# Kernel optimization log

Measured on AMD Instinct MI355X. Metric: run time of the kernel, lower is better.

Reference implementation:

```python
import jax, jax.numpy as jnp
import numpy as np
from jax import lax

B, L, DIN, DOUT, K = 8, 4096, 256, 256, 3


def _gates(x, W, b, k):
    # x: [B, L, Din] -> conv over time, channels-first like torch Conv1d
    xt = jnp.transpose(x, (0, 2, 1))  # [B, Din, L]
    pad = (k - 1) // 2
    g = lax.conv_general_dilated(xt, W, window_strides=(1,), padding=[(pad, pad)],
                                 dimension_numbers=("NCH", "OIH", "NCH"))
    g = g + b[None, :, None]
    g = jnp.transpose(g, (0, 2, 1))  # [B, L, 3*Dout]
    f, o, z = jnp.split(g, 3, axis=-1)
    return jax.nn.sigmoid(f), jax.nn.sigmoid(o), jnp.tanh(z)


def _fo_pool(f, z, init_cell, reverse):
    # c_t = f_t * c_{t-1} + (1 - f_t) * z_t ; scan over time axis
    fT = jnp.transpose(f, (1, 0, 2))  # [L, B, D]
    zT = jnp.transpose(z, (1, 0, 2))

    def step(c, fz):
        ft, zt = fz
        c = ft * c + (1.0 - ft) * zt
        return c, c

    _, cells = lax.scan(step, init_cell, (fT, zT), reverse=reverse)
    return jnp.transpose(cells, (1, 0, 2))  # [B, L, D]


def setup_inputs() -> dict:
    key = jax.random.key(0)
    k1, k2, k3, k4, k5, k6 = jax.random.split(key, 6)
    scale_in = 1.0 / np.sqrt(DIN * K)
    inp = {
        "input": jax.random.normal(k1, (B, L, DIN), dtype=jnp.float32),
        "lengths": jnp.full((B,), L, dtype=jnp.int64) if False else jax.random.randint(k2, (B,), 1, L + 1),
        "W_fwd": jax.random.uniform(k3, (3 * DOUT, DIN, K), dtype=jnp.float32, minval=-scale_in, maxval=scale_in),
        "b_fwd": jax.random.uniform(k4, (3 * DOUT,), dtype=jnp.float32, minval=-scale_in, maxval=scale_in),
        "W_bwd": jax.random.uniform(k5, (3 * DOUT, DIN, K), dtype=jnp.float32, minval=-scale_in, maxval=scale_in),
        "b_bwd": jax.random.uniform(k6, (3 * DOUT,), dtype=jnp.float32, minval=-scale_in, maxval=scale_in),
    }
    return inp


def reference(input, lengths, W_fwd, b_fwd, W_bwd, b_bwd):
    init_cell = jnp.zeros((input.shape[0], DOUT), dtype=input.dtype)

    # forward direction
    f, o, z = _gates(input, W_fwd, b_fwd, K)
    cell = _fo_pool(f, z, init_cell, reverse=False)
    hidden = cell * o

    # backward direction
    fr, orr, zr = _gates(input, W_bwd, b_bwd, K)
    rcell = _fo_pool(fr, zr, init_cell, reverse=True)
    rhidden = rcell * orr

    output = jnp.concatenate([hidden, rhidden], axis=-1)  # [B, L, 2*Dout]
    last_h = jnp.concatenate([hidden[:, -1, :], rhidden[:, -1, :]], axis=-1)
    last_c = jnp.concatenate([cell[:, -1, :], rcell[:, -1, :]], axis=-1)
    return output, last_h, last_c
```

## Files before the change

kernel.cpp:

```cpp
#include <hip/hip_runtime.h>
#include <hip/hip_bf16.h>
#include <hip/hip_fp16.h>

#define B_     8
#define L_     4096
#define DIN    256
#define DOUT   256
#define NGATE  1536
#define KDIM   768
#define LP     (L_ + 2)
#define CHUNK  64
#define NCHUNK (L_ / CHUNK)

typedef short  short8  __attribute__((ext_vector_type(8)));
typedef __bf16 bf16x8  __attribute__((ext_vector_type(8)));
typedef float  floatx4 __attribute__((ext_vector_type(4)));

__device__ __forceinline__ float fast_sigmoid(float x) {
    return __builtin_amdgcn_rcpf(1.f + __expf(-x));
}
__device__ __forceinline__ float fast_tanh(float x) {
    return 1.f - 2.f * __builtin_amdgcn_rcpf(1.f + __expf(2.f * x));
}
__device__ __forceinline__ unsigned short f2bf(float x) {
    unsigned u = __float_as_uint(x);
    u += 0x7FFF + ((u >> 16) & 1);
    return (unsigned short)(u >> 16);
}
__device__ __forceinline__ void gload16(const unsigned short* g, unsigned short* l) {
    __builtin_amdgcn_global_load_lds((const __attribute__((address_space(1))) void*)g,
                                     (__attribute__((address_space(3))) void*)l,
                                     16, 0, 0);
}

__global__ void prep_x(const float* __restrict__ x, unsigned short* __restrict__ Xp) {
    int idx = blockIdx.x * 256 + threadIdx.x;
    int row = idx >> 6;
    if (row >= B_ * LP) return;
    int c4 = (idx & 63) << 2;
    int b = row / LP, r = row - b * LP;
    float4 v = make_float4(0.f, 0.f, 0.f, 0.f);
    if (r >= 1 && r <= L_) {
        v = *(const float4*)(x + ((size_t)(b * L_ + (r - 1))) * DIN + c4);
    }
    ushort4 o = make_ushort4(f2bf(v.x), f2bf(v.y), f2bf(v.z), f2bf(v.w));
    *(ushort4*)(Xp + (size_t)row * DIN + c4) = o;
}

__global__ void prep_w(const float* __restrict__ Wf, const float* __restrict__ bf_,
                       const float* __restrict__ Wb, const float* __restrict__ bb,
                       unsigned short* __restrict__ Wc, float* __restrict__ bc) {
    int gid = blockIdx.x * 256 + threadIdx.x;
    if (gid < NGATE) {
        bc[gid] = (gid < 768) ? bf_[gid] : bb[gid - 768];
    }
    if (gid >= NGATE * KDIM) return;
    int n = gid / KDIM, k = gid - n * KDIM;
    int s = k >> 8, ic = k & 255;
    const float* W = (n < 768) ? Wf : Wb;
    int oc = (n < 768) ? n : n - 768;
    float v = W[(size_t)oc * KDIM + ic * 3 + s];
    Wc[(size_t)n * KDIM + k] = f2bf(v);
}

__launch_bounds__(256)
__global__ void gemm_gates(const unsigned short* __restrict__ Xp,
                           const unsigned short* __restrict__ Wc,
                           const float* __restrict__ bc,
                           _Float16* __restrict__ gates) {
    __shared__ unsigned short As[128 * 64];
    __shared__ unsigned short Bs[128 * 64];
    const int tid  = threadIdx.x;
    const int lane = tid & 63, wave = tid >> 6;
    const int quad = lane >> 4, l16 = lane & 15;
    const int wr = wave >> 1, wcl = wave & 1;

    int flat = blockIdx.x;
    int xcd  = flat & 7;
    int slot = flat >> 3;
    int m    = xcd * 32 + slot / 12;
    int nblk = slot % 12;
    const int b  = m >> 5;
    const int t0 = (m & 31) << 7;
    const int n0 = nblk << 7;
    const unsigned short* Ab = Xp + (size_t)b * LP * DIN;

    int rowj[4], cgj[4];
#pragma unroll
    for (int j = 0; j < 4; j++) {
        int G = (wave * 4 + j) * 64 + lane;
        rowj[j] = G >> 3;
        cgj[j]  = ((G & 7) ^ (rowj[j] & 7)) * 8;
    }

    floatx4 acc[4][4];
#pragma unroll
    for (int i = 0; i < 4; i++)
#pragma unroll
        for (int j = 0; j < 4; j++) acc[i][j] = (floatx4)0.f;

    for (int k0 = 0; k0 < KDIM; k0 += 64) {
        const int sh = k0 >> 8;
        const int c0 = k0 & 255;
#pragma unroll
        for (int j = 0; j < 4; j++) {
            gload16(Ab + (size_t)(t0 + rowj[j] + sh) * DIN + c0 + cgj[j],
                    &As[(wave * 4 + j) * 512]);
            gload16(Wc + (size_t)(n0 + rowj[j]) * KDIM + k0 + cgj[j],
                    &Bs[(wave * 4 + j) * 512]);
        }
        __syncthreads();
#pragma unroll
        for (int kk = 0; kk < 2; kk++) {
            const int g0 = kk * 4 + quad;
            short8 af[4], bfr[4];
#pragma unroll
            for (int mi = 0; mi < 4; mi++) {
                int row = wr * 64 + mi * 16 + l16;
                af[mi] = *(const short8*)&As[row * 64 + ((g0 ^ (row & 7)) << 3)];
            }
#pragma unroll
            for (int ni = 0; ni < 4; ni++) {
                int row = wcl * 64 + ni * 16 + l16;
                bfr[ni] = *(const short8*)&Bs[row * 64 + ((g0 ^ (row & 7)) << 3)];
            }
#pragma unroll
            for (int mi = 0; mi < 4; mi++)
#pragma unroll
                for (int ni = 0; ni < 4; ni++)
                    acc[mi][ni] = __builtin_amdgcn_mfma_f32_16x16x32_bf16(
                        __builtin_bit_cast(bf16x8, af[mi]),
                        __builtin_bit_cast(bf16x8, bfr[ni]),
                        acc[mi][ni], 0, 0, 0);
        }
        __syncthreads();
    }

#pragma unroll
    for (int ni = 0; ni < 4; ni++) {
        int col = wcl * 64 + ni * 16 + l16;
        int n = n0 + col;
        float bias = bc[n];
        int cls = (n >> 8) % 3;
#pragma unroll
        for (int mi = 0; mi < 4; mi++) {
#pragma unroll
            for (int rr = 0; rr < 4; rr++) {
                int row = wr * 64 + mi * 16 + quad * 4 + rr;
                float v = acc[mi][ni][rr] + bias;
                v = (cls == 2) ? fast_tanh(v) : fast_sigmoid(v);
                gates[((size_t)(b * L_ + t0 + row)) * NGATE + n] = (_Float16)v;
            }
        }
    }
}

__global__ void scan_chunks(const __half2* __restrict__ gates2,
                            float2* __restrict__ PW) {
    const int tid = threadIdx.x;
    const int dd = tid & 127, sub = tid >> 7;
    const int s = blockIdx.x * 2 + sub, b = blockIdx.y, dir = blockIdx.z;
    const __half2* gb = gates2 + (size_t)(b * L_) * (NGATE / 2) + dir * 384 + dd;
    float2 P = make_float2(1.f, 1.f), W = make_float2(0.f, 0.f);
    if (dir == 0) {
        int t = s * CHUNK;
        for (int i = 0; i < CHUNK; i++, t++) {
            const __half2* g = gb + (size_t)t * (NGATE / 2);
            float2 f = __half22float2(g[0]);
            float2 z = __half22float2(g[256]);
            W.x = f.x * W.x + (1.f - f.x) * z.x;
            W.y = f.y * W.y + (1.f - f.y) * z.y;
            P.x *= f.x; P.y *= f.y;
        }
    } else {
        int t = s * CHUNK + CHUNK - 1;
        for (int i = 0; i < CHUNK; i++, t--) {
            const __half2* g = gb + (size_t)t * (NGATE / 2);
            float2 f = __half22float2(g[0]);
            float2 z = __half22float2(g[256]);
            W.x = f.x * W.x + (1.f - f.x) * z.x;
            W.y = f.y * W.y + (1.f - f.y) * z.y;
            P.x *= f.x; P.y *= f.y;
        }
    }
    float4 o4 = make_float4(P.x, W.x, P.y, W.y);
    *(float4*)&PW[(((size_t)(dir * 8 + b) * NCHUNK + s) * 256) + 2 * dd] = o4;
}

__global__ void scan_seq(const float2* __restrict__ PW, float* __restrict__ C0) {
    const int c = threadIdx.x;
    const int dir = blockIdx.x >> 3, b = blockIdx.x & 7;
    const size_t base = ((size_t)(dir * 8 + b)) * NCHUNK * 256 + c;
    float cc = 0.f;
    if (dir == 0) {
#pragma unroll
        for (int s = 0; s < NCHUNK; s++) {
            float2 pw = PW[base + (size_t)s * 256];
            C0[base + (size_t)s * 256] = cc;
            cc = pw.x * cc + pw.y;
        }
    } else {
#pragma unroll
        for (int s = NCHUNK - 1; s >= 0; s--) {
            float2 pw = PW[base + (size_t)s * 256];
            C0[base + (size_t)s * 256] = cc;
            cc = pw.x * cc + pw.y;
        }
    }
}

__global__ void scan_final(const __half2* __restrict__ gates2,
                           const float* __restrict__ C0,
                           float* __restrict__ out) {
    const int tid = threadIdx.x;
    const int dd = tid & 127, sub = tid >> 7;
    const int s = blockIdx.x * 2 + sub, b = blockIdx.y, dir = blockIdx.z;
    const __half2* gb = gates2 + (size_t)(b * L_) * (NGATE / 2) + dir * 384 + dd;
    float2 c = *(const float2*)&C0[(((size_t)(dir * 8 + b) * NCHUNK + s) * 256) + 2 * dd];
    float* ob = out + (size_t)(b * L_) * (2 * DOUT) + dir * DOUT + 2 * dd;
    float* lasth = out + (size_t)B_ * L_ * (2 * DOUT);
    float* lastc = lasth + B_ * (2 * DOUT);
    if (dir == 0) {
        int t = s * CHUNK;
        for (int i = 0; i < CHUNK; i++, t++) {
            const __half2* g = gb + (size_t)t * (NGATE / 2);
            float2 f = __half22float2(g[0]);
            float2 o = __half22float2(g[128]);
            float2 z = __half22float2(g[256]);
            c.x = f.x * c.x + (1.f - f.x) * z.x;
            c.y = f.y * c.y + (1.f - f.y) * z.y;
            float2 h = make_float2(c.x * o.x, c.y * o.y);
            *(float2*)&ob[(size_t)t * (2 * DOUT)] = h;
            if (t == L_ - 1) {
                *(float2*)&lasth[b * 2 * DOUT + 2 * dd] = h;
                *(float2*)&lastc[b * 2 * DOUT + 2 * dd] = c;
            }
        }
    } else {
        int t = s * CHUNK + CHUNK - 1;
        for (int i = 0; i < CHUNK; i++, t--) {
            const __half2* g = gb + (size_t)t * (NGATE / 2);
            float2 f = __half22float2(g[0]);
            float2 o = __half22float2(g[128]);
            float2 z = __half22float2(g[256]);
            c.x = f.x * c.x + (1.f - f.x) * z.x;
            c.y = f.y * c.y + (1.f - f.y) * z.y;
            float2 h = make_float2(c.x * o.x, c.y * o.y);
            *(float2*)&ob[(size_t)t * (2 * DOUT)] = h;
            if (t == L_ - 1) {
                *(float2*)&lasth[b * 2 * DOUT + DOUT + 2 * dd] = h;
                *(float2*)&lastc[b * 2 * DOUT + DOUT + 2 * dd] = c;
            }
        }
    }
}

extern "C" void kernel_launch(void* const* d_in, const int* in_sizes, int n_in,
                              void* d_out, int out_size, void* d_ws, size_t ws_size,
                              hipStream_t stream) {
    const float* x   = (const float*)d_in[0];
    const float* Wf  = (const float*)d_in[2];
    const float* bfv = (const float*)d_in[3];
    const float* Wb  = (const float*)d_in[4];
    const float* bbv = (const float*)d_in[5];

    char* ws = (char*)d_ws;
    unsigned short* Xp    = (unsigned short*)(ws);
    unsigned short* Wc    = (unsigned short*)(ws + 16785408);
    float*          bc    = (float*)(ws + 19144704);
    _Float16*       gates = (_Float16*)(ws + 19150848);
    float2*         PW    = (float2*)(ws + 119814144);
    float*          C0    = (float*)(ws + 121911296);
    float*          out   = (float*)d_out;

    prep_x<<<(B_ * LP * 64 + 255) / 256, 256, 0, stream>>>(x, Xp);
    prep_w<<<(NGATE * KDIM + 255) / 256, 256, 0, stream>>>(Wf, bfv, Wb, bbv, Wc, bc);
    gemm_gates<<<3072, 256, 0, stream>>>(Xp, Wc, bc, gates);
    scan_chunks<<<dim3(NCHUNK / 2, B_, 2), 256, 0, stream>>>((const __half2*)gates, PW);
    scan_seq<<<16, 256, 0, stream>>>(PW, C0);
    scan_final<<<dim3(NCHUNK / 2, B_, 2), 256, 0, stream>>>((const __half2*)gates, C0, out);
}
```

Baseline: 252.3 us.

## Enlarge GEMM M-tile to 256, vectorize scans with half4, halve chunk size

The gate GEMM now uses 512-thread blocks with a 256-row A tile sharing each 128-column B tile, which halves weight reloads per output. The chunked scan kernels have each thread handle 4 channels through half4 loads and float4 stores, and CHUNK drops to 32 to expose more parallel chunks. PW and C0 now alias the Xp workspace region, which is dead by the time the scans run. The cost is higher register and LDS pressure in the GEMM, and a longer sequential scan_seq pass.

```diff
diff --git a/kernel.cpp b/kernel.cpp
--- a/kernel.cpp
+++ b/kernel.cpp
@@ -9,12 +9,13 @@
 #define NGATE  1536
 #define KDIM   768
 #define LP     (L_ + 2)
-#define CHUNK  64
+#define CHUNK  32
 #define NCHUNK (L_ / CHUNK)
 
-typedef short  short8  __attribute__((ext_vector_type(8)));
-typedef __bf16 bf16x8  __attribute__((ext_vector_type(8)));
-typedef float  floatx4 __attribute__((ext_vector_type(4)));
+typedef short    short8  __attribute__((ext_vector_type(8)));
+typedef __bf16   bf16x8  __attribute__((ext_vector_type(8)));
+typedef float    floatx4 __attribute__((ext_vector_type(4)));
+typedef _Float16 half4   __attribute__((ext_vector_type(4)));
 
 __device__ __forceinline__ float fast_sigmoid(float x) {
     return __builtin_amdgcn_rcpf(1.f + __expf(-x));
@@ -63,12 +64,12 @@
     Wc[(size_t)n * KDIM + k] = f2bf(v);
 }
 
-__launch_bounds__(256)
+__launch_bounds__(512)
 __global__ void gemm_gates(const unsigned short* __restrict__ Xp,
                            const unsigned short* __restrict__ Wc,
                            const float* __restrict__ bc,
                            _Float16* __restrict__ gates) {
-    __shared__ unsigned short As[128 * 64];
+    __shared__ unsigned short As[256 * 64];
     __shared__ unsigned short Bs[128 * 64];
     const int tid  = threadIdx.x;
     const int lane = tid & 63, wave = tid >> 6;
@@ -78,19 +79,25 @@
     int flat = blockIdx.x;
     int xcd  = flat & 7;
     int slot = flat >> 3;
-    int m    = xcd * 32 + slot / 12;
+    int m    = xcd * 16 + slot / 12;
     int nblk = slot % 12;
-    const int b  = m >> 5;
-    const int t0 = (m & 31) << 7;
+    const int b  = m >> 4;
+    const int t0 = (m & 15) << 8;
     const int n0 = nblk << 7;
     const unsigned short* Ab = Xp + (size_t)b * LP * DIN;
 
-    int rowj[4], cgj[4];
+    int rowA[4], cgA[4], rowB[2], cgB[2];
 #pragma unroll
     for (int j = 0; j < 4; j++) {
         int G = (wave * 4 + j) * 64 + lane;
-        rowj[j] = G >> 3;
-        cgj[j]  = ((G & 7) ^ (rowj[j] & 7)) * 8;
+        rowA[j] = G >> 3;
+        cgA[j]  = ((G & 7) ^ (rowA[j] & 7)) * 8;
+    }
+#pragma unroll
+    for (int j = 0; j < 2; j++) {
+        int G = (wave * 2 + j) * 64 + lane;
+        rowB[j] = G >> 3;
+        cgB[j]  = ((G & 7) ^ (rowB[j] & 7)) * 8;
     }
 
     floatx4 acc[4][4];
@@ -103,12 +110,13 @@
         const int sh = k0 >> 8;
         const int c0 = k0 & 255;
 #pragma unroll
-        for (int j = 0; j < 4; j++) {
-            gload16(Ab + (size_t)(t0 + rowj[j] + sh) * DIN + c0 + cgj[j],
+        for (int j = 0; j < 4; j++)
+            gload16(Ab + (size_t)(t0 + rowA[j] + sh) * DIN + c0 + cgA[j],
                     &As[(wave * 4 + j) * 512]);
-            gload16(Wc + (size_t)(n0 + rowj[j]) * KDIM + k0 + cgj[j],
-                    &Bs[(wave * 4 + j) * 512]);
-        }
+#pragma unroll
+        for (int j = 0; j < 2; j++)
+            gload16(Wc + (size_t)(n0 + rowB[j]) * KDIM + k0 + cgB[j],
+                    &Bs[(wave * 2 + j) * 512]);
         __syncthreads();
 #pragma unroll
         for (int kk = 0; kk < 2; kk++) {
@@ -155,36 +163,45 @@
     }
 }
 
-__global__ void scan_chunks(const __half2* __restrict__ gates2,
+__global__ void scan_chunks(const _Float16* __restrict__ gates,
                             float2* __restrict__ PW) {
     const int tid = threadIdx.x;
-    const int dd = tid & 127, sub = tid >> 7;
-    const int s = blockIdx.x * 2 + sub, b = blockIdx.y, dir = blockIdx.z;
-    const __half2* gb = gates2 + (size_t)(b * L_) * (NGATE / 2) + dir * 384 + dd;
-    float2 P = make_float2(1.f, 1.f), W = make_float2(0.f, 0.f);
+    const int cg = tid & 63, sub = tid >> 6;
+    const int s = blockIdx.x * 4 + sub, b = blockIdx.y, dir = blockIdx.z;
+    const _Float16* gb = gates + (size_t)(b * L_) * NGATE + dir * 768 + cg * 4;
+    float P[4] = {1.f, 1.f, 1.f, 1.f}, W[4] = {0.f, 0.f, 0.f, 0.f};
     if (dir == 0) {
         int t = s * CHUNK;
+#pragma unroll 8
         for (int i = 0; i < CHUNK; i++, t++) {
-            const __half2* g = gb + (size_t)t * (NGATE / 2);
-            float2 f = __half22float2(g[0]);
-            float2 z = __half22float2(g[256]);
-            W.x = f.x * W.x + (1.f - f.x) * z.x;
-            W.y = f.y * W.y + (1.f - f.y) * z.y;
-            P.x *= f.x; P.y *= f.y;
+            half4 f4 = *(const half4*)(gb + (size_t)t * NGATE);
+            half4 z4 = *(const half4*)(gb + (size_t)t * NGATE + 512);
+#pragma unroll
+            for (int u = 0; u < 4; u++) {
+                float f = (float)f4[u], z = (float)z4[u];
+                W[u] = f * W[u] + (1.f - f) * z;
+                P[u] *= f;
+            }
         }
     } else {
         int t = s * CHUNK + CHUNK - 1;
+#pragma unroll 8
         for (int i = 0; i < CHUNK; i++, t--) {
-            const __half2* g = gb + (size_t)t * (NGATE / 2);
-            float2 f = __half22float2(g[0]);
-            float2 z = __half22float2(g[256]);
-            W.x = f.x * W.x + (1.f - f.x) * z.x;
-            W.y = f.y * W.y + (1.f - f.y) * z.y;
-            P.x *= f.x; P.y *= f.y;
-        }
-    }
-    float4 o4 = make_float4(P.x, W.x, P.y, W.y);
-    *(float4*)&PW[(((size_t)(dir * 8 + b) * NCHUNK + s) * 256) + 2 * dd] = o4;
+            half4 f4 = *(const half4*)(gb + (size_t)t * NGATE);
+            half4 z4 = *(const half4*)(gb + (size_t)t * NGATE + 512);
+#pragma unroll
+            for (int u = 0; u < 4; u++) {
+                float f = (float)f4[u], z = (float)z4[u];
+                W[u] = f * W[u] + (1.f - f) * z;
+                P[u] *= f;
+            }
+        }
+    }
+    float2* p = &PW[(((size_t)(dir * 8 + b)) * NCHUNK + s) * 256 + cg * 4];
+    float4 o0 = make_float4(P[0], W[0], P[1], W[1]);
+    float4 o1 = make_float4(P[2], W[2], P[3], W[3]);
+    *(float4*)&p[0] = o0;
+    *(float4*)&p[2] = o1;
 }
 
 __global__ void scan_seq(const float2* __restrict__ PW, float* __restrict__ C0) {
@@ -193,14 +210,14 @@
     const size_t base = ((size_t)(dir * 8 + b)) * NCHUNK * 256 + c;
     float cc = 0.f;
     if (dir == 0) {
-#pragma unroll
+#pragma unroll 16
         for (int s = 0; s < NCHUNK; s++) {
             float2 pw = PW[base + (size_t)s * 256];
             C0[base + (size_t)s * 256] = cc;
             cc = pw.x * cc + pw.y;
         }
     } else {
-#pragma unroll
+#pragma unroll 16
         for (int s = NCHUNK - 1; s >= 0; s--) {
             float2 pw = PW[base + (size_t)s * 256];
             C0[base + (size_t)s * 256] = cc;
@@ -209,48 +226,39 @@
     }
 }
 
-__global__ void scan_final(const __half2* __restrict__ gates2,
+__global__ void scan_final(const _Float16* __restrict__ gates,
                            const float* __restrict__ C0,
                            float* __restrict__ out) {
     const int tid = threadIdx.x;
-    const int dd = tid & 127, sub = tid >> 7;
-    const int s = blockIdx.x * 2 + sub, b = blockIdx.y, dir = blockIdx.z;
-    const __half2* gb = gates2 + (size_t)(b * L_) * (NGATE / 2) + dir * 384 + dd;
-    float2 c = *(const float2*)&C0[(((size_t)(dir * 8 + b) * NCHUNK + s) * 256) + 2 * dd];
-    float* ob = out + (size_t)(b * L_) * (2 * DOUT) + dir * DOUT + 2 * dd;
+    const int cg = tid & 63, sub = tid >> 6;
+    const int s = blockIdx.x * 4 + sub, b = blockIdx.y, dir = blockIdx.z;
+    const _Float16* gb = gates + (size_t)(b * L_) * NGATE + dir * 768 + cg * 4;
+    float4 c = *(const float4*)&C0[(((size_t)(dir * 8 + b)) * NCHUNK + s) * 256 + cg * 4];
+    float* ob = out + (size_t)(b * L_) * (2 * DOUT) + dir * DOUT + cg * 4;
     float* lasth = out + (size_t)B_ * L_ * (2 * DOUT);
     float* lastc = lasth + B_ * (2 * DOUT);
-    if (dir == 0) {
-        int t = s * CHUNK;
-        for (int i = 0; i < CHUNK; i++, t++) {
-            const __half2* g = gb + (size_t)t * (NGATE / 2);
-            float2 f = __half22float2(g[0]);
-            float2 o = __half22float2(g[128]);
-            float2 z = __half22float2(g[256]);
-            c.x = f.x * c.x + (1.f - f.x) * z.x;
-            c.y = f.y * c.y + (1.f - f.y) * z.y;
-            float2 h = make_float2(c.x * o.x, c.y * o.y);
-            *(float2*)&ob[(size_t)t * (2 * DOUT)] = h;
-            if (t == L_ - 1) {
-                *(float2*)&lasth[b * 2 * DOUT + 2 * dd] = h;
-                *(float2*)&lastc[b * 2 * DOUT + 2 * dd] = c;
-            }
-        }
-    } else {
-        int t = s * CHUNK + CHUNK - 1;
-        for (int i = 0; i < CHUNK; i++, t--) {
-            const __half2* g = gb + (size_t)t * (NGATE / 2);
-            float2 f = __half22float2(g[0]);
-            float2 o = __half22float2(g[128]);
-            float2 z = __half22float2(g[256]);
-            c.x = f.x * c.x + (1.f - f.x) * z.x;
-            c.y = f.y * c.y + (1.f - f.y) * z.y;
-            float2 h = make_float2(c.x * o.x, c.y * o.y);
-            *(float2*)&ob[(size_t)t * (2 * DOUT)] = h;
-            if (t == L_ - 1) {
-                *(float2*)&lasth[b * 2 * DOUT + DOUT + 2 * dd] = h;
-                *(float2*)&lastc[b * 2 * DOUT + DOUT + 2 * dd] = c;
-            }
+    const int step = (dir == 0) ? 1 : -1;
+    int t = (dir == 0) ? s * CHUNK : s * CHUNK + CHUNK - 1;
+#pragma unroll 8
+    for (int i = 0; i < CHUNK; i++, t += step) {
+        half4 f4 = *(const half4*)(gb + (size_t)t * NGATE);
+        half4 o4 = *(const half4*)(gb + (size_t)t * NGATE + 256);
+        half4 z4 = *(const half4*)(gb + (size_t)t * NGATE + 512);
+        float4 h;
+        {
+            float f = (float)f4[0], z = (float)z4[0];
+            c.x = f * c.x + (1.f - f) * z; h.x = c.x * (float)o4[0];
+            f = (float)f4[1]; z = (float)z4[1];
+            c.y = f * c.y + (1.f - f) * z; h.y = c.y * (float)o4[1];
+            f = (float)f4[2]; z = (float)z4[2];
+            c.z = f * c.z + (1.f - f) * z; h.z = c.z * (float)o4[2];
+            f = (float)f4[3]; z = (float)z4[3];
+            c.w = f * c.w + (1.f - f) * z; h.w = c.w * (float)o4[3];
+        }
+        *(float4*)&ob[(size_t)t * (2 * DOUT)] = h;
+        if (t == L_ - 1) {
+            *(float4*)&lasth[b * 2 * DOUT + dir * DOUT + cg * 4] = h;
+            *(float4*)&lastc[b * 2 * DOUT + dir * DOUT + cg * 4] = c;
         }
     }
 }
@@ -269,14 +277,14 @@
     unsigned short* Wc    = (unsigned short*)(ws + 16785408);
     float*          bc    = (float*)(ws + 19144704);
     _Float16*       gates = (_Float16*)(ws + 19150848);
-    float2*         PW    = (float2*)(ws + 119814144);
-    float*          C0    = (float*)(ws + 121911296);
+    float2*         PW    = (float2*)(ws);
+    float*          C0    = (float*)(ws + 4194304);
     float*          out   = (float*)d_out;
 
     prep_x<<<(B_ * LP * 64 + 255) / 256, 256, 0, stream>>>(x, Xp);
     prep_w<<<(NGATE * KDIM + 255) / 256, 256, 0, stream>>>(Wf, bfv, Wb, bbv, Wc, bc);
-    gemm_gates<<<3072, 256, 0, stream>>>(Xp, Wc, bc, gates);
-    scan_chunks<<<dim3(NCHUNK / 2, B_, 2), 256, 0, stream>>>((const __half2*)gates, PW);
+    gemm_gates<<<1536, 512, 0, stream>>>(Xp, Wc, bc, gates);
+    scan_chunks<<<dim3(NCHUNK / 4, B_, 2), 256, 0, stream>>>(gates, PW);
     scan_seq<<<16, 256, 0, stream>>>(PW, C0);
-    scan_final<<<dim3(NCHUNK / 2, B_, 2), 256, 0, stream>>>((const __half2*)gates, C0, out);
-}
+    scan_final<<<dim3(NCHUNK / 4, B_, 2), 256, 0, stream>>>(gates, C0, out);
+}
```

After: 232.5 us. 7.8% less time.
